# Performance work log

Hardware: AMD Instinct MI355X
Metric: run time of the kernel (lower is better)

Reference implementation:

```python
import jax, jax.numpy as jnp
import numpy as np

NUM_NODES = 100000
IN_CH = 128
OUT_CH = 64
NUM_EDGES = 1000000


def setup_inputs() -> dict:
    key = jax.random.key(0)
    ks = jax.random.split(key, 16)

    x = jax.random.normal(ks[0], (NUM_NODES, IN_CH), dtype=jnp.float32)

    def make_edges(k_src, k_tgt, k_w):
        src = jax.random.randint(k_src, (NUM_EDGES,), 0, NUM_NODES, dtype=jnp.int32)
        # tf.math.segment_sum requires sorted segment ids -> sort targets
        tgt = jnp.sort(jax.random.randint(k_tgt, (NUM_EDGES,), 0, NUM_NODES, dtype=jnp.int32))
        ei = jnp.stack([src, tgt], axis=0)  # (2, E)
        ew = jax.random.uniform(k_w, (NUM_EDGES,), dtype=jnp.float32)
        return ei, ew

    edge_index_in, edge_weight_in = make_edges(ks[1], ks[2], ks[3])
    edge_index_out, edge_weight_out = make_edges(ks[4], ks[5], ks[6])

    glorot = (6.0 / (IN_CH + OUT_CH)) ** 0.5
    W_main_in = jax.random.uniform(ks[7], (IN_CH, OUT_CH), minval=-glorot, maxval=glorot, dtype=jnp.float32)
    W_main_out = jax.random.uniform(ks[8], (IN_CH, OUT_CH), minval=-glorot, maxval=glorot, dtype=jnp.float32)
    W_shared = jax.random.uniform(ks[9], (IN_CH, OUT_CH), minval=-glorot, maxval=glorot, dtype=jnp.float32)

    bias_main_in = jnp.zeros((OUT_CH,), dtype=jnp.float32)
    bias_main_out = jnp.zeros((OUT_CH,), dtype=jnp.float32)
    bias_shared_in = jnp.zeros((OUT_CH,), dtype=jnp.float32)
    bias_shared_out = jnp.zeros((OUT_CH,), dtype=jnp.float32)

    C_in_vec = jnp.ones((NUM_NODES, 1), dtype=jnp.float32)
    C_out_vec = jnp.ones((NUM_NODES, 1), dtype=jnp.float32)

    return {
        "x": x,
        "W_main_in": W_main_in,
        "W_main_out": W_main_out,
        "W_shared": W_shared,
        "bias_main_in": bias_main_in,
        "bias_main_out": bias_main_out,
        "bias_shared_in": bias_shared_in,
        "bias_shared_out": bias_shared_out,
        "C_in_vec": C_in_vec,
        "C_out_vec": C_out_vec,
        "edge_index_in": edge_index_in,
        "edge_weight_in": edge_weight_in,
        "edge_index_out": edge_index_out,
        "edge_weight_out": edge_weight_out,
    }


def _propagate(h, edge_index, edge_weight, num_nodes):
    # gather messages from source nodes, scale by edge weight, sum into targets
    src = edge_index[0]
    tgt = edge_index[1]
    msgs = h[src] * edge_weight[:, None]  # (E, OUT_CH)
    return jax.ops.segment_sum(msgs, tgt, num_segments=num_nodes)  # (N, OUT_CH)


def reference(x, W_main_in, W_main_out, W_shared,
              bias_main_in, bias_main_out, bias_shared_in, bias_shared_out,
              C_in_vec, C_out_vec,
              edge_index_in, edge_weight_in, edge_index_out, edge_weight_out):
    n = x.shape[0]
    h_main_in = _propagate(x @ W_main_in, edge_index_in, edge_weight_in, n)
    h_shared_in = _propagate(x @ W_shared, edge_index_in, edge_weight_in, n)
    ic_combined = h_main_in + bias_main_in + (h_shared_in + bias_shared_in)

    h_main_out = _propagate(x @ W_main_out, edge_index_out, edge_weight_out, n)
    h_shared_out = _propagate(x @ W_shared, edge_index_out, edge_weight_out, n)
    oc_combined = h_main_out + bias_main_out + (h_shared_out + bias_shared_out)

    return C_in_vec * ic_combined + C_out_vec * oc_combined
```

## Files before the change

### kernel.cpp

```cpp
#include <hip/hip_runtime.h>

#define IN_CH   128
#define OUT_CH  64
#define M_TILE  128
#define XS_PITCH 136

typedef __attribute__((ext_vector_type(8))) short short8;
typedef __attribute__((ext_vector_type(4))) float floatx4;

__device__ __forceinline__ unsigned short f2bf(float f) {
    union { float f; unsigned u; } v; v.f = f;
    unsigned r = v.u + 0x7fffu + ((v.u >> 16) & 1u);
    return (unsigned short)(r >> 16);
}
__device__ __forceinline__ float bfl(unsigned u) {
    return __uint_as_float(u << 16);
}
__device__ __forceinline__ float bfh(unsigned u) {
    return __uint_as_float(u & 0xffff0000u);
}

__global__ void prep_kernel(const int* __restrict__ tgtIn,
                            const int* __restrict__ tgtOut,
                            const float* __restrict__ Wmi,
                            const float* __restrict__ Wmo,
                            const float* __restrict__ Wsh,
                            int* __restrict__ rpIn,
                            int* __restrict__ rpOut,
                            unsigned short* __restrict__ WcT,
                            int n_nodes, int neIn, int neOut)
{
    int i = blockIdx.x * blockDim.x + threadIdx.x;
    int half = n_nodes + 1;
    if (i < 2 * half) {
        const int* tgt; int* rp; int t; int ne;
        if (i < half) { tgt = tgtIn;  rp = rpIn;  t = i;        ne = neIn; }
        else          { tgt = tgtOut; rp = rpOut; t = i - half; ne = neOut; }
        int lo = 0, hi = ne;
        while (lo < hi) {
            int mid = (lo + hi) >> 1;
            if (tgt[mid] < t) lo = mid + 1; else hi = mid;
        }
        rp[t] = lo;
    } else {
        int j = i - 2 * half;
        if (j < 2 * OUT_CH * IN_CH) {
            int n = j >> 7, k = j & 127;
            float m = (n < OUT_CH) ? Wmi[k * OUT_CH + n]
                                   : Wmo[k * OUT_CH + (n - OUT_CH)];
            float s = Wsh[k * OUT_CH + (n & (OUT_CH - 1))];
            WcT[n * IN_CH + k] = f2bf(m + s);
        }
    }
}

__global__ __launch_bounds__(256, 3)
void gemm_kernel(const float* __restrict__ x,
                 const unsigned short* __restrict__ WcT,
                 unsigned short* __restrict__ Abf,
                 unsigned short* __restrict__ Bbf,
                 int n_nodes)
{
    __shared__ unsigned short Xs[M_TILE][XS_PITCH];

    const int tid  = threadIdx.x;
    const int w    = tid >> 6;
    const int lane = tid & 63;
    const int l15  = lane & 15;
    const int quad = lane >> 4;
    const long long node0 = (long long)blockIdx.x * M_TILE;

    short8 bfrag[4][2];
#pragma unroll
    for (int ks = 0; ks < 4; ++ks)
#pragma unroll
        for (int ni = 0; ni < 2; ++ni)
            bfrag[ks][ni] = *(const short8*)&WcT[(w * 32 + ni * 16 + l15) * IN_CH
                                                 + ks * 32 + quad * 8];

    {
        const float4* x4 = (const float4*)x;
        for (int i = tid; i < M_TILE * (IN_CH / 4); i += 256) {
            int row = i >> 5, c4 = i & 31;
            long long node = node0 + row;
            float4 v = make_float4(0.f, 0.f, 0.f, 0.f);
            if (node < n_nodes) v = x4[node * (IN_CH / 4) + c4];
            uint2 p;
            p.x = ((unsigned)f2bf(v.y) << 16) | f2bf(v.x);
            p.y = ((unsigned)f2bf(v.w) << 16) | f2bf(v.z);
            *(uint2*)&Xs[row][c4 * 4] = p;
        }
    }
    __syncthreads();

    floatx4 acc[8][2];
#pragma unroll
    for (int mi = 0; mi < 8; ++mi)
#pragma unroll
        for (int ni = 0; ni < 2; ++ni)
            acc[mi][ni] = (floatx4){0.f, 0.f, 0.f, 0.f};

#pragma unroll
    for (int ks = 0; ks < 4; ++ks) {
        const int k0 = ks * 32 + quad * 8;
#pragma unroll
        for (int mi = 0; mi < 8; ++mi) {
            short8 a = *(const short8*)&Xs[mi * 16 + l15][k0];
            acc[mi][0] = __builtin_amdgcn_mfma_f32_16x16x32_bf16(a, bfrag[ks][0], acc[mi][0], 0, 0, 0);
            acc[mi][1] = __builtin_amdgcn_mfma_f32_16x16x32_bf16(a, bfrag[ks][1], acc[mi][1], 0, 0, 0);
        }
    }

    unsigned short* Hout = (w < 2) ? Abf : Bbf;
    const int colb = (w & 1) * 32;
#pragma unroll
    for (int mi = 0; mi < 8; ++mi)
#pragma unroll
        for (int ni = 0; ni < 2; ++ni)
#pragma unroll
            for (int r = 0; r < 4; ++r) {
                long long row = node0 + mi * 16 + quad * 4 + r;
                if (row < n_nodes)
                    Hout[row * OUT_CH + colb + ni * 16 + l15] = f2bf(acc[mi][ni][r]);
            }
}

__global__ __launch_bounds__(256)
void prop_kernel(const unsigned short* __restrict__ H,
                 const int* __restrict__ rpIn, const int* __restrict__ rpOut,
                 const int* __restrict__ srcIn, const float* __restrict__ ewIn,
                 const int* __restrict__ srcOut, const float* __restrict__ ewOut,
                 const float* __restrict__ bmi, const float* __restrict__ bmo,
                 const float* __restrict__ bsi, const float* __restrict__ bso,
                 const float* __restrict__ Cin, const float* __restrict__ Cout,
                 float* __restrict__ out, int n_nodes, int neIn, int neOut)
{
    const int lane = threadIdx.x & 63;
    const int wv   = threadIdx.x >> 6;
    const int e    = lane >> 3;
    const int el   = lane & 7;
    const int ch8  = el * 8;
    const int eb   = lane & 56;

    const unsigned short* Hq = H + ch8;

    const int t = ((int)blockIdx.x * 4 + wv) * 8 + e;
    const bool valid = (t < n_nodes);
    const int tc = valid ? t : 0;

    const int Boff = n_nodes * OUT_CH;

    int ei0 = rpIn[tc],  ei1 = rpIn[tc + 1];
    int eo0 = rpOut[tc], eo1 = rpOut[tc + 1];
    int dIn  = ei1 - ei0;
    int len  = valid ? (dIn + (eo1 - eo0)) : 0;
    float ci = Cin[tc], co = Cout[tc];

    int ml = len;
    ml = max(ml, __shfl_xor(ml, 8));
    ml = max(ml, __shfl_xor(ml, 16));
    ml = max(ml, __shfl_xor(ml, 32));
    const int maxlen = __builtin_amdgcn_readfirstlane(ml);

    float a0 = 0.f, a1 = 0.f, a2 = 0.f, a3 = 0.f;
    float a4 = 0.f, a5 = 0.f, a6 = 0.f, a7 = 0.f;

    auto load_raw = [&](int j, int& sI, float& wI, int& sO, float& wO) {
        int iIn  = min(ei0 + max(0, min(j, dIn - 1)), neIn - 1);
        int jo   = j - dIn;
        int iOut = min(eo0 + max(0, jo), neOut - 1);
        sI = srcIn[iIn];  wI = ewIn[iIn];
        sO = srcOut[iOut]; wO = ewOut[iOut];
    };

    int   sI, sO;  float wI, wO;
    load_raw(el, sI, wI, sO, wO);

    for (int p = 0; p < maxlen; p += 8) {
        int j = p + el;
        bool inSeg  = (j < dIn);
        bool anySeg = (j < len);
        int   rowb = inSeg ? (sI * OUT_CH) : (sO * OUT_CH + Boff);
        rowb = anySeg ? rowb : 0;
        float wj = inSeg ? (ci * wI) : (anySeg ? (co * wO) : 0.f);

        if (p + 8 < maxlen)
            load_raw(p + 8 + el, sI, wI, sO, wO);

        int   r0 = __shfl(rowb, eb + 0), r1 = __shfl(rowb, eb + 1);
        int   r2 = __shfl(rowb, eb + 2), r3 = __shfl(rowb, eb + 3);
        int   r4 = __shfl(rowb, eb + 4), r5 = __shfl(rowb, eb + 5);
        int   r6 = __shfl(rowb, eb + 6), r7 = __shfl(rowb, eb + 7);
        float w0 = __shfl(wj, eb + 0), w1 = __shfl(wj, eb + 1);
        float w2 = __shfl(wj, eb + 2), w3 = __shfl(wj, eb + 3);
        float w4 = __shfl(wj, eb + 4), w5 = __shfl(wj, eb + 5);
        float w6 = __shfl(wj, eb + 6), w7 = __shfl(wj, eb + 7);
        uint4 u0 = *(const uint4*)(Hq + r0);
        uint4 u1 = *(const uint4*)(Hq + r1);
        uint4 u2 = *(const uint4*)(Hq + r2);
        uint4 u3 = *(const uint4*)(Hq + r3);
        uint4 u4 = *(const uint4*)(Hq + r4);
        uint4 u5 = *(const uint4*)(Hq + r5);
        uint4 u6 = *(const uint4*)(Hq + r6);
        uint4 u7 = *(const uint4*)(Hq + r7);
        a0 += w0 * bfl(u0.x); a1 += w0 * bfh(u0.x); a2 += w0 * bfl(u0.y); a3 += w0 * bfh(u0.y);
        a4 += w0 * bfl(u0.z); a5 += w0 * bfh(u0.z); a6 += w0 * bfl(u0.w); a7 += w0 * bfh(u0.w);
        a0 += w1 * bfl(u1.x); a1 += w1 * bfh(u1.x); a2 += w1 * bfl(u1.y); a3 += w1 * bfh(u1.y);
        a4 += w1 * bfl(u1.z); a5 += w1 * bfh(u1.z); a6 += w1 * bfl(u1.w); a7 += w1 * bfh(u1.w);
        a0 += w2 * bfl(u2.x); a1 += w2 * bfh(u2.x); a2 += w2 * bfl(u2.y); a3 += w2 * bfh(u2.y);
        a4 += w2 * bfl(u2.z); a5 += w2 * bfh(u2.z); a6 += w2 * bfl(u2.w); a7 += w2 * bfh(u2.w);
        a0 += w3 * bfl(u3.x); a1 += w3 * bfh(u3.x); a2 += w3 * bfl(u3.y); a3 += w3 * bfh(u3.y);
        a4 += w3 * bfl(u3.z); a5 += w3 * bfh(u3.z); a6 += w3 * bfl(u3.w); a7 += w3 * bfh(u3.w);
        a0 += w4 * bfl(u4.x); a1 += w4 * bfh(u4.x); a2 += w4 * bfl(u4.y); a3 += w4 * bfh(u4.y);
        a4 += w4 * bfl(u4.z); a5 += w4 * bfh(u4.z); a6 += w4 * bfl(u4.w); a7 += w4 * bfh(u4.w);
        a0 += w5 * bfl(u5.x); a1 += w5 * bfh(u5.x); a2 += w5 * bfl(u5.y); a3 += w5 * bfh(u5.y);
        a4 += w5 * bfl(u5.z); a5 += w5 * bfh(u5.z); a6 += w5 * bfl(u5.w); a7 += w5 * bfh(u5.w);
        a0 += w6 * bfl(u6.x); a1 += w6 * bfh(u6.x); a2 += w6 * bfl(u6.y); a3 += w6 * bfh(u6.y);
        a4 += w6 * bfl(u6.z); a5 += w6 * bfh(u6.z); a6 += w6 * bfl(u6.w); a7 += w6 * bfh(u6.w);
        a0 += w7 * bfl(u7.x); a1 += w7 * bfh(u7.x); a2 += w7 * bfl(u7.y); a3 += w7 * bfh(u7.y);
        a4 += w7 * bfl(u7.z); a5 += w7 * bfh(u7.z); a6 += w7 * bfl(u7.w); a7 += w7 * bfh(u7.w);
    }

    if (valid) {
        float4 o0, o1;
        o0.x = a0 + ci * (bmi[ch8 + 0] + bsi[ch8 + 0]) + co * (bmo[ch8 + 0] + bso[ch8 + 0]);
        o0.y = a1 + ci * (bmi[ch8 + 1] + bsi[ch8 + 1]) + co * (bmo[ch8 + 1] + bso[ch8 + 1]);
        o0.z = a2 + ci * (bmi[ch8 + 2] + bsi[ch8 + 2]) + co * (bmo[ch8 + 2] + bso[ch8 + 2]);
        o0.w = a3 + ci * (bmi[ch8 + 3] + bsi[ch8 + 3]) + co * (bmo[ch8 + 3] + bso[ch8 + 3]);
        o1.x = a4 + ci * (bmi[ch8 + 4] + bsi[ch8 + 4]) + co * (bmo[ch8 + 4] + bso[ch8 + 4]);
        o1.y = a5 + ci * (bmi[ch8 + 5] + bsi[ch8 + 5]) + co * (bmo[ch8 + 5] + bso[ch8 + 5]);
        o1.z = a6 + ci * (bmi[ch8 + 6] + bsi[ch8 + 6]) + co * (bmo[ch8 + 6] + bso[ch8 + 6]);
        o1.w = a7 + ci * (bmi[ch8 + 7] + bsi[ch8 + 7]) + co * (bmo[ch8 + 7] + bso[ch8 + 7]);
        float* ob = out + (long long)t * OUT_CH + ch8;
        *(float4*)ob = o0;
        *(float4*)(ob + 4) = o1;
    }
}

extern "C" void kernel_launch(void* const* d_in, const int* in_sizes, int n_in,
                              void* d_out, int out_size, void* d_ws, size_t ws_size,
                              hipStream_t stream)
{
    const float* x    = (const float*)d_in[0];
    const float* Wmi  = (const float*)d_in[1];
    const float* Wmo  = (const float*)d_in[2];
    const float* Wsh  = (const float*)d_in[3];
    const float* bmi  = (const float*)d_in[4];
    const float* bmo  = (const float*)d_in[5];
    const float* bsi  = (const float*)d_in[6];
    const float* bso  = (const float*)d_in[7];
    const float* Cin  = (const float*)d_in[8];
    const float* Cout = (const float*)d_in[9];
    const int*   eiIn  = (const int*)d_in[10];
    const float* ewIn  = (const float*)d_in[11];
    const int*   eiOut = (const int*)d_in[12];
    const float* ewOut = (const float*)d_in[13];

    const int n_nodes = in_sizes[0] / IN_CH;
    const int neIn  = in_sizes[11];
    const int neOut = in_sizes[13];

    const int* srcIn  = eiIn;
    const int* tgtIn  = eiIn + neIn;
    const int* srcOut = eiOut;
    const int* tgtOut = eiOut + neOut;

    char* ws = (char*)d_ws;
    size_t NH = (size_t)n_nodes * OUT_CH * sizeof(unsigned short);
    unsigned short* Abf = (unsigned short*)ws;
    unsigned short* Bbf = (unsigned short*)(ws + NH);
    int* rpIn  = (int*)(ws + 2 * NH);
    int* rpOut = rpIn + (n_nodes + 1);
    unsigned short* WcT = (unsigned short*)(rpOut + (n_nodes + 1));

    int prep_threads = 2 * (n_nodes + 1) + 2 * OUT_CH * IN_CH;
    prep_kernel<<<(prep_threads + 255) / 256, 256, 0, stream>>>(
        tgtIn, tgtOut, Wmi, Wmo, Wsh, rpIn, rpOut, WcT, n_nodes, neIn, neOut);

    int gblocks = (n_nodes + M_TILE - 1) / M_TILE;
    gemm_kernel<<<gblocks, 256, 0, stream>>>(x, WcT, Abf, Bbf, n_nodes);

    int pblocks = (n_nodes + 31) / 32;
    prop_kernel<<<pblocks, 256, 0, stream>>>(
        Abf, rpIn, rpOut, srcIn, ewIn, srcOut, ewOut,
        bmi, bmo, bsi, bso, Cin, Cout, (float*)d_out, n_nodes, neIn, neOut);
}
```

Baseline: 187.4 us.

## Build CSR row pointers per edge, stage GEMM output via LDS, raise prop occupancy

```diff
diff --git a/kernel.cpp b/kernel.cpp
--- a/kernel.cpp
+++ b/kernel.cpp
@@ -31,19 +31,22 @@
                             int n_nodes, int neIn, int neOut)
 {
     int i = blockIdx.x * blockDim.x + threadIdx.x;
-    int half = n_nodes + 1;
-    if (i < 2 * half) {
-        const int* tgt; int* rp; int t; int ne;
-        if (i < half) { tgt = tgtIn;  rp = rpIn;  t = i;        ne = neIn; }
-        else          { tgt = tgtOut; rp = rpOut; t = i - half; ne = neOut; }
-        int lo = 0, hi = ne;
-        while (lo < hi) {
-            int mid = (lo + hi) >> 1;
-            if (tgt[mid] < t) lo = mid + 1; else hi = mid;
-        }
-        rp[t] = lo;
+    const int nIn1 = neIn + 1, nOut1 = neOut + 1;
+
+    if (i < nIn1 + nOut1) {
+        const int* tgt; int* rp; int idx; int ne;
+        if (i < nIn1) { tgt = tgtIn;  rp = rpIn;  idx = i;        ne = neIn; }
+        else          { tgt = tgtOut; rp = rpOut; idx = i - nIn1; ne = neOut; }
+        if (idx < ne) {
+            int a    = tgt[idx];
+            int prev = (idx == 0) ? -1 : tgt[idx - 1];
+            for (int t = prev + 1; t <= a; ++t) rp[t] = idx;
+        } else {
+            int last = (ne > 0) ? tgt[ne - 1] : -1;
+            for (int t = last + 1; t <= n_nodes; ++t) rp[t] = ne;
+        }
     } else {
-        int j = i - 2 * half;
+        int j = i - (nIn1 + nOut1);
         if (j < 2 * OUT_CH * IN_CH) {
             int n = j >> 7, k = j & 127;
             float m = (n < OUT_CH) ? Wmi[k * OUT_CH + n]
@@ -111,21 +114,32 @@
         }
     }
 
-    unsigned short* Hout = (w < 2) ? Abf : Bbf;
-    const int colb = (w & 1) * 32;
+    __syncthreads();
+    const int colb = w * 32;
 #pragma unroll
     for (int mi = 0; mi < 8; ++mi)
 #pragma unroll
         for (int ni = 0; ni < 2; ++ni)
 #pragma unroll
-            for (int r = 0; r < 4; ++r) {
-                long long row = node0 + mi * 16 + quad * 4 + r;
-                if (row < n_nodes)
-                    Hout[row * OUT_CH + colb + ni * 16 + l15] = f2bf(acc[mi][ni][r]);
-            }
-}
-
-__global__ __launch_bounds__(256)
+            for (int r = 0; r < 4; ++r)
+                Xs[mi * 16 + quad * 4 + r][colb + ni * 16 + l15] =
+                    f2bf(acc[mi][ni][r]);
+    __syncthreads();
+
+    for (int i = tid; i < M_TILE * 16; i += 256) {
+        int row  = i >> 4;
+        int half = (i >> 3) & 1;
+        int v4   = i & 7;
+        long long node = node0 + row;
+        if (node < n_nodes) {
+            uint4 v = *(const uint4*)&Xs[row][half * 64 + v4 * 8];
+            unsigned short* dst = half ? Bbf : Abf;
+            *(uint4*)&dst[node * OUT_CH + v4 * 8] = v;
+        }
+    }
+}
+
+__global__ __launch_bounds__(256, 8)
 void prop_kernel(const unsigned short* __restrict__ H,
                  const int* __restrict__ rpIn, const int* __restrict__ rpOut,
                  const int* __restrict__ srcIn, const float* __restrict__ ewIn,
@@ -273,7 +287,7 @@
     int* rpOut = rpIn + (n_nodes + 1);
     unsigned short* WcT = (unsigned short*)(rpOut + (n_nodes + 1));
 
-    int prep_threads = 2 * (n_nodes + 1) + 2 * OUT_CH * IN_CH;
+    int prep_threads = (neIn + 1) + (neOut + 1) + 2 * OUT_CH * IN_CH;
     prep_kernel<<<(prep_threads + 255) / 256, 256, 0, stream>>>(
         tgtIn, tgtOut, Wmi, Wmo, Wsh, rpIn, rpOut, WcT, n_nodes, neIn, neOut);
 
```

After: 321.9 us. +71.8%, slower.
